# Optimization experiments

Hardware: AMD Instinct MI355X
Metric: run time of the kernel (lower is better)

The kernel has to match this reference:

```python
import jax, jax.numpy as jnp
import numpy as np

N = 50000        # node_num
E = 1600000      # num edges (avg degree 32)
IN_DIM = 128
OUT_DIM = 64
SLOPE = 0.1      # leaky relu slope_ratio
EPS = 1e-12


def setup_inputs() -> dict:
    key = jax.random.key(0)
    k0, k1, k2, k3 = jax.random.split(key, 4)
    x = jax.random.normal(k0, (N, IN_DIM), dtype=jnp.float32)
    edge_index = jax.random.randint(k1, (2, E), 0, N, dtype=jnp.int64)
    # Linear(in_dim, out_dim) params
    W = jax.random.normal(k2, (OUT_DIM, IN_DIM), dtype=jnp.float32) * (1.0 / np.sqrt(IN_DIM))
    b = jnp.zeros((OUT_DIM,), dtype=jnp.float32)
    # attention vector a: [2*out_dim, 1], kaiming-normal-ish init
    a = jax.random.normal(k3, (2 * OUT_DIM, 1), dtype=jnp.float32) * np.sqrt(2.0 / (2 * OUT_DIM))
    return {"x": x, "edge_index": edge_index, "W": W, "b": b, "a": a}


def reference(x, edge_index, W, b, a):
    # new_embeddings = Linear(x)
    new = x @ W.T + b                          # [N, OUT_DIM]
    src = edge_index[0]
    dst = edge_index[1]
    # cat(new[src], new[dst]) @ a  ==  new[src]@a_src + new[dst]@a_dst (avoids [E, 2*OUT] intermediate)
    a_src = a[:OUT_DIM, 0]                     # [OUT_DIM]
    a_dst = a[OUT_DIM:, 0]                     # [OUT_DIM]
    score = new[src] @ a_src + new[dst] @ a_dst  # [E]
    e = jnp.exp(jax.nn.leaky_relu(score, SLOPE))  # [E]
    # spmm(A, ones) -> per-row sum of edge weights; spmm(A, new) -> weighted aggregation
    row_sum = jax.ops.segment_sum(e, src, num_segments=N)                 # [N]
    results = jax.ops.segment_sum(e[:, None] * new[dst], src, num_segments=N)  # [N, OUT_DIM]
    return results / (row_sum[:, None] + EPS)
```

## Files before the change

### kernel.cpp

```cpp
#include <hip/hip_runtime.h>
#include <hip/hip_bf16.h>

#define NN    50000
#define EE    1600000
#define IND   128
#define OUTD  64
#define SLOPE 0.1f

#define BSH    5
#define BW     32
#define NB     1564
#define NFINE  1568
#define CAP    1408
#define CAPT   6
#define CSH    8
#define NC     196
#define CAP1   8832
#define NBLK1  500
#define CHUNK1 (EE / NBLK1)
#define NSPLIT 4
#define SCAP   (CAP1 / NSPLIT)
#define NLIN   (NN / 16)

typedef __attribute__((ext_vector_type(8))) short short8;
typedef __attribute__((ext_vector_type(4))) float float4v;

union SMem {
    struct {
        ushort xs[16 * 136];
        ushort wt[64 * 136];
        float  newt[16 * 68];
    } lin;
    int h[NC];
};

__global__ __launch_bounds__(256) void fused_lincoarse_kernel(
    const float* __restrict__ x, const float* __restrict__ W,
    const float* __restrict__ bias, const float* __restrict__ a,
    const int* __restrict__ ei, int* __restrict__ gcur1,
    unsigned* __restrict__ ebuf1,
    ushort* __restrict__ nbuf2, float* __restrict__ s_src, float* __restrict__ s_dst)
{
    __shared__ SMem sm;
    const int tid = threadIdx.x;

    if (blockIdx.x < NBLK1) {
        int* h = sm.h;
        for (int i = tid; i < NC; i += 256) h[i] = 0;
        __syncthreads();
        const int base = blockIdx.x * CHUNK1;
        const int4* s4p = (const int4*)(ei + base);
        for (int i = tid; i < CHUNK1 / 4; i += 256) {
            int4 s4 = s4p[i];
            atomicAdd(&h[s4.x >> CSH], 1);
            atomicAdd(&h[s4.y >> CSH], 1);
            atomicAdd(&h[s4.z >> CSH], 1);
            atomicAdd(&h[s4.w >> CSH], 1);
        }
        __syncthreads();
        for (int i = tid; i < NC; i += 256) {
            int c = h[i];
            if (c) h[i] = i * CAP1 + atomicAdd(&gcur1[i * 16], c);
        }
        __syncthreads();
        const int4* d4p = (const int4*)(ei + EE + base);
        for (int i = tid; i < CHUNK1 / 4; i += 256) {
            int4 s4 = s4p[i];
            int4 d4 = d4p[i];
            int p0 = atomicAdd(&h[s4.x >> CSH], 1);
            int p1 = atomicAdd(&h[s4.y >> CSH], 1);
            int p2 = atomicAdd(&h[s4.z >> CSH], 1);
            int p3 = atomicAdd(&h[s4.w >> CSH], 1);
            ebuf1[p0] = ((unsigned)(s4.x & 255) << 16) | (unsigned)d4.x;
            ebuf1[p1] = ((unsigned)(s4.y & 255) << 16) | (unsigned)d4.y;
            ebuf1[p2] = ((unsigned)(s4.z & 255) << 16) | (unsigned)d4.z;
            ebuf1[p3] = ((unsigned)(s4.w & 255) << 16) | (unsigned)d4.w;
        }
        return;
    }

    const int node0 = (blockIdx.x - NBLK1) * 16;
    const float4* W4 = (const float4*)W;
    #pragma unroll
    for (int i = 0; i < 8; ++i) {
        int idx = tid + i * 256;
        float4 wv = W4[idx];
        int n = idx >> 5, k = (idx & 31) * 4;
        ushort4 pk; __hip_bfloat16 h;
        h = __float2bfloat16(wv.x); pk.x = *(ushort*)&h;
        h = __float2bfloat16(wv.y); pk.y = *(ushort*)&h;
        h = __float2bfloat16(wv.z); pk.z = *(ushort*)&h;
        h = __float2bfloat16(wv.w); pk.w = *(ushort*)&h;
        *(ushort4*)&sm.lin.wt[n * 136 + k] = pk;
    }
    const float4* x4 = (const float4*)(x + (size_t)node0 * IND);
    #pragma unroll
    for (int i = 0; i < 2; ++i) {
        int idx = tid + i * 256;
        float4 xv = x4[idx];
        int r = idx >> 5, cc = (idx & 31) * 4;
        ushort4 pk; __hip_bfloat16 h;
        h = __float2bfloat16(xv.x); pk.x = *(ushort*)&h;
        h = __float2bfloat16(xv.y); pk.y = *(ushort*)&h;
        h = __float2bfloat16(xv.z); pk.z = *(ushort*)&h;
        h = __float2bfloat16(xv.w); pk.w = *(ushort*)&h;
        *(ushort4*)&sm.lin.xs[r * 136 + cc] = pk;
    }
    __syncthreads();

    const int w    = tid >> 6;
    const int lane = tid & 63;
    const int q    = lane >> 4;
    const int m16  = lane & 15;
    float4v acc = {0.f, 0.f, 0.f, 0.f};
    #pragma unroll
    for (int kk = 0; kk < IND; kk += 32) {
        short8 af = *(const short8*)&sm.lin.xs[m16 * 136 + kk + q * 8];
        short8 bf = *(const short8*)&sm.lin.wt[(w * 16 + m16) * 136 + kk + q * 8];
        acc = __builtin_amdgcn_mfma_f32_16x16x32_bf16(af, bf, acc, 0, 0, 0);
    }
    const float bv = bias[w * 16 + m16];
    #pragma unroll
    for (int r = 0; r < 4; ++r)
        sm.lin.newt[(q * 4 + r) * 68 + w * 16 + m16] = acc[r] + bv;
    __syncthreads();

    const int nl = tid >> 4;
    const int jg = tid & 15;
    const int j0 = jg * 4;
    float4 va = *(const float4*)&sm.lin.newt[nl * 68 + j0];
    const int n = node0 + nl;
    ushort4 pk;
    { __hip_bfloat16 h;
      h = __float2bfloat16(va.x); pk.x = *(ushort*)&h;
      h = __float2bfloat16(va.y); pk.y = *(ushort*)&h;
      h = __float2bfloat16(va.z); pk.z = *(ushort*)&h;
      h = __float2bfloat16(va.w); pk.w = *(ushort*)&h; }
    *(ushort4*)&nbuf2[(size_t)n * OUTD + j0] = pk;

    float ss = va.x * a[j0]        + va.y * a[j0 + 1]
             + va.z * a[j0 + 2]    + va.w * a[j0 + 3];
    float sd = va.x * a[OUTD + j0]     + va.y * a[OUTD + j0 + 1]
             + va.z * a[OUTD + j0 + 2] + va.w * a[OUTD + j0 + 3];
    #pragma unroll
    for (int m = 1; m < 16; m <<= 1) {
        ss += __shfl_xor(ss, m, 64);
        sd += __shfl_xor(sd, m, 64);
    }
    if (jg == 0) { s_src[n] = ss; s_dst[n] = sd; }
}

__global__ __launch_bounds__(256) void finebin_kernel(
    const unsigned* __restrict__ ebuf1, const int* __restrict__ gcur1,
    int* __restrict__ gcur2, unsigned* __restrict__ ebuf2)
{
    __shared__ unsigned stage[SCAP];
    __shared__ int h[8], lofs[8], grun[8], cur[8];
    const int tid = threadIdx.x;
    const int c   = blockIdx.x >> 2;
    const int sp  = blockIdx.x & 3;
    const int cnt1 = gcur1[c * 16];
    const int seg  = (cnt1 + NSPLIT - 1) / NSPLIT;
    const int lo   = sp * seg;
    const int m    = max(0, min(cnt1, lo + seg) - lo);
    if (tid < 8) h[tid] = 0;
    __syncthreads();
    const unsigned* eb = ebuf1 + (size_t)c * CAP1 + lo;
    for (int i = tid; i < m; i += 256)
        atomicAdd(&h[eb[i] >> 21], 1);
    __syncthreads();
    if (tid == 0) {
        int run = 0;
        #pragma unroll
        for (int f = 0; f < 8; ++f) { lofs[f] = run; run += h[f]; }
    }
    __syncthreads();
    if (tid < 8) {
        cur[tid]  = lofs[tid];
        grun[tid] = atomicAdd(&gcur2[(c * 8 + tid) * 16], h[tid]);
    }
    __syncthreads();
    for (int i = tid; i < m; i += 256) {
        unsigned e = eb[i];
        int pos = atomicAdd(&cur[e >> 21], 1);
        stage[pos] = (((e >> 16) & 31u) << 16) | (e & 0xFFFFu);
    }
    __syncthreads();
    #pragma unroll 1
    for (int f = 0; f < 8; ++f) {
        const int cf = h[f];
        unsigned* dst = ebuf2 + (size_t)(c * 8 + f) * CAP + grun[f];
        const unsigned* sp2 = stage + lofs[f];
        for (int i = tid; i < cf; i += 256) dst[i] = sp2[i];
    }
}

__global__ __launch_bounds__(256) void aggregate_kernel(
    const unsigned* __restrict__ ebuf, const int* __restrict__ gcur,
    const ushort* __restrict__ nbuf2,
    const float* __restrict__ s_src, const float* __restrict__ s_dst,
    float* __restrict__ out)
{
    __shared__ uint2 pairs[CAP];
    __shared__ float ssL[BW];
    __shared__ int cntL[BW], ofs[BW], cur[BW];
    const int tid  = threadIdx.x;
    const int wid  = tid >> 6;
    const int lane = tid & 63;
    const int b    = blockIdx.x;
    const int n0   = b << BSH;
    const uint2* __restrict__ nbufq = (const uint2*)nbuf2;

    if (tid < BW) {
        int n = n0 + tid;
        ssL[tid]  = (n < NN) ? s_src[n] : 0.f;
        cntL[tid] = 0;
    }
    __syncthreads();

    const int cnt = gcur[b * 16];
    const unsigned* eb = ebuf + (size_t)b * CAP;

    unsigned er[CAPT]; float evr[CAPT];
    int nk = 0;
    for (int i = tid; i < cnt; i += 256) {
        unsigned e = eb[i];
        int d  = e & 0xFFFFu;
        int ln = e >> 16;
        float sc = ssL[ln] + s_dst[d];
        float lr = sc > 0.f ? sc : SLOPE * sc;
        er[nk] = e; evr[nk] = __expf(lr); ++nk;
        atomicAdd(&cntL[ln], 1);
    }
    __syncthreads();

    if (wid == 0) {
        int c = (lane < BW) ? cntL[lane] : 0;
        int sc = c;
        #pragma unroll
        for (int m = 1; m < BW; m <<= 1) {
            int v = __shfl_up(sc, m, 64);
            if (lane >= m) sc += v;
        }
        if (lane < BW) { ofs[lane] = sc - c; cur[lane] = sc - c; }
    }
    __syncthreads();

    for (int k = 0; k < nk; ++k) {
        int ln = er[k] >> 16;
        int pos = atomicAdd(&cur[ln], 1);
        pairs[pos] = make_uint2(er[k] & 0xFFFFu, __float_as_uint(evr[k]));
    }
    __syncthreads();

    const int e16 = lane >> 4;
    const int c16 = lane & 15;

    #pragma unroll 1
    for (int t = 0; t < BW / 4; ++t) {
        const int ln  = wid * (BW / 4) + t;
        const int beg = ofs[ln];
        const int len = cntL[ln];

        float a0 = 0.f, a1 = 0.f, a2 = 0.f, a3 = 0.f, es = 0.f;
        int j = 0;
        for (; j + 16 <= len; j += 16) {
            uint2 pA = pairs[beg + j + 0  + e16];
            uint2 pB = pairs[beg + j + 4  + e16];
            uint2 pC = pairs[beg + j + 8  + e16];
            uint2 pD = pairs[beg + j + 12 + e16];
            uint2 gA = nbufq[pA.x * 16 + c16];
            uint2 gB = nbufq[pB.x * 16 + c16];
            uint2 gC = nbufq[pC.x * 16 + c16];
            uint2 gD = nbufq[pD.x * 16 + c16];
            float fA = __uint_as_float(pA.y), fB = __uint_as_float(pB.y);
            float fC = __uint_as_float(pC.y), fD = __uint_as_float(pD.y);
            es += fA + fB + fC + fD;
            a0 = fmaf(fA, __uint_as_float(gA.x << 16), a0);
            a1 = fmaf(fA, __uint_as_float(gA.x & 0xFFFF0000u), a1);
            a2 = fmaf(fA, __uint_as_float(gA.y << 16), a2);
            a3 = fmaf(fA, __uint_as_float(gA.y & 0xFFFF0000u), a3);
            a0 = fmaf(fB, __uint_as_float(gB.x << 16), a0);
            a1 = fmaf(fB, __uint_as_float(gB.x & 0xFFFF0000u), a1);
            a2 = fmaf(fB, __uint_as_float(gB.y << 16), a2);
            a3 = fmaf(fB, __uint_as_float(gB.y & 0xFFFF0000u), a3);
            a0 = fmaf(fC, __uint_as_float(gC.x << 16), a0);
            a1 = fmaf(fC, __uint_as_float(gC.x & 0xFFFF0000u), a1);
            a2 = fmaf(fC, __uint_as_float(gC.y << 16), a2);
            a3 = fmaf(fC, __uint_as_float(gC.y & 0xFFFF0000u), a3);
            a0 = fmaf(fD, __uint_as_float(gD.x << 16), a0);
            a1 = fmaf(fD, __uint_as_float(gD.x & 0xFFFF0000u), a1);
            a2 = fmaf(fD, __uint_as_float(gD.y << 16), a2);
            a3 = fmaf(fD, __uint_as_float(gD.y & 0xFFFF0000u), a3);
        }
        for (; j < len; j += 4) {
            int idx = j + e16;
            uint2 p = pairs[beg + min(idx, len - 1)];
            float f = (idx < len) ? __uint_as_float(p.y) : 0.f;
            uint2 g = nbufq[p.x * 16 + c16];
            es += f;
            a0 = fmaf(f, __uint_as_float(g.x << 16), a0);
            a1 = fmaf(f, __uint_as_float(g.x & 0xFFFF0000u), a1);
            a2 = fmaf(f, __uint_as_float(g.y << 16), a2);
            a3 = fmaf(f, __uint_as_float(g.y & 0xFFFF0000u), a3);
        }
        es += __shfl_xor(es, 16, 64); es += __shfl_xor(es, 32, 64);
        a0 += __shfl_xor(a0, 16, 64); a0 += __shfl_xor(a0, 32, 64);
        a1 += __shfl_xor(a1, 16, 64); a1 += __shfl_xor(a1, 32, 64);
        a2 += __shfl_xor(a2, 16, 64); a2 += __shfl_xor(a2, 32, 64);
        a3 += __shfl_xor(a3, 16, 64); a3 += __shfl_xor(a3, 32, 64);
        const int n = n0 + ln;
        if (e16 == 0 && n < NN) {
            float inv = 1.f / (es + 1e-12f);
            float4 o = make_float4(a0 * inv, a1 * inv, a2 * inv, a3 * inv);
            *(float4*)&out[(size_t)n * OUTD + c16 * 4] = o;
        }
    }
}

extern "C" void kernel_launch(void* const* d_in, const int* in_sizes, int n_in,
                              void* d_out, int out_size, void* d_ws, size_t ws_size,
                              hipStream_t stream) {
    const float* x  = (const float*)d_in[0];
    const int*   ei = (const int*)d_in[1];
    const float* W  = (const float*)d_in[2];
    const float* b  = (const float*)d_in[3];
    const float* a  = (const float*)d_in[4];
    float* out = (float*)d_out;

    ushort*   nbuf2 = (ushort*)d_ws;
    float*    s_src = (float*)(nbuf2 + (size_t)NN * OUTD);
    float*    s_dst = s_src + NN;
    int*      gcur1 = (int*)(s_dst + NN);
    int*      gcur2 = gcur1 + NC * 16;
    unsigned* ebuf1 = (unsigned*)(gcur2 + NFINE * 16);
    unsigned* ebuf2 = ebuf1 + (size_t)NC * CAP1;

    hipMemsetAsync(gcur1, 0, (NC + NFINE) * 16 * sizeof(int), stream);
    fused_lincoarse_kernel<<<NBLK1 + NLIN, 256, 0, stream>>>(
        x, W, b, a, ei, gcur1, ebuf1, nbuf2, s_src, s_dst);
    finebin_kernel<<<NC * NSPLIT, 256, 0, stream>>>(ebuf1, gcur1, gcur2, ebuf2);
    aggregate_kernel<<<NB, 256, 0, stream>>>(ebuf2, gcur2, nbuf2, s_src, s_dst, out);
}
```

Before: 146.6 us.

## Fold fine binning into aggregation by filtering coarse bins per block

Removes the separate fine-binning kernel and its intermediate edge buffer. Each aggregation block now scans the whole coarse bin (eight blocks' worth of edges) twice and keeps only edges matching its sub-bin. This saves one launch, one global write and read of the edge buffer, and a memset, at the cost of reading each coarse bin eight times over and doing redundant filtering work per block.

Measured after the change: 156.6 us. 6.8% more time.

```diff
diff --git a/kernel.cpp b/kernel.cpp
--- a/kernel.cpp
+++ b/kernel.cpp
@@ -10,16 +10,12 @@
 #define BSH    5
 #define BW     32
 #define NB     1564
-#define NFINE  1568
 #define CAP    1408
-#define CAPT   6
 #define CSH    8
 #define NC     196
 #define CAP1   8832
 #define NBLK1  500
 #define CHUNK1 (EE / NBLK1)
-#define NSPLIT 4
-#define SCAP   (CAP1 / NSPLIT)
 #define NLIN   (NN / 16)
 
 typedef __attribute__((ext_vector_type(8))) short short8;
@@ -150,53 +146,8 @@
     if (jg == 0) { s_src[n] = ss; s_dst[n] = sd; }
 }
 
-__global__ __launch_bounds__(256) void finebin_kernel(
+__global__ __launch_bounds__(256) void aggregate_kernel(
     const unsigned* __restrict__ ebuf1, const int* __restrict__ gcur1,
-    int* __restrict__ gcur2, unsigned* __restrict__ ebuf2)
-{
-    __shared__ unsigned stage[SCAP];
-    __shared__ int h[8], lofs[8], grun[8], cur[8];
-    const int tid = threadIdx.x;
-    const int c   = blockIdx.x >> 2;
-    const int sp  = blockIdx.x & 3;
-    const int cnt1 = gcur1[c * 16];
-    const int seg  = (cnt1 + NSPLIT - 1) / NSPLIT;
-    const int lo   = sp * seg;
-    const int m    = max(0, min(cnt1, lo + seg) - lo);
-    if (tid < 8) h[tid] = 0;
-    __syncthreads();
-    const unsigned* eb = ebuf1 + (size_t)c * CAP1 + lo;
-    for (int i = tid; i < m; i += 256)
-        atomicAdd(&h[eb[i] >> 21], 1);
-    __syncthreads();
-    if (tid == 0) {
-        int run = 0;
-        #pragma unroll
-        for (int f = 0; f < 8; ++f) { lofs[f] = run; run += h[f]; }
-    }
-    __syncthreads();
-    if (tid < 8) {
-        cur[tid]  = lofs[tid];
-        grun[tid] = atomicAdd(&gcur2[(c * 8 + tid) * 16], h[tid]);
-    }
-    __syncthreads();
-    for (int i = tid; i < m; i += 256) {
-        unsigned e = eb[i];
-        int pos = atomicAdd(&cur[e >> 21], 1);
-        stage[pos] = (((e >> 16) & 31u) << 16) | (e & 0xFFFFu);
-    }
-    __syncthreads();
-    #pragma unroll 1
-    for (int f = 0; f < 8; ++f) {
-        const int cf = h[f];
-        unsigned* dst = ebuf2 + (size_t)(c * 8 + f) * CAP + grun[f];
-        const unsigned* sp2 = stage + lofs[f];
-        for (int i = tid; i < cf; i += 256) dst[i] = sp2[i];
-    }
-}
-
-__global__ __launch_bounds__(256) void aggregate_kernel(
-    const unsigned* __restrict__ ebuf, const int* __restrict__ gcur,
     const ushort* __restrict__ nbuf2,
     const float* __restrict__ s_src, const float* __restrict__ s_dst,
     float* __restrict__ out)
@@ -208,6 +159,8 @@
     const int wid  = tid >> 6;
     const int lane = tid & 63;
     const int b    = blockIdx.x;
+    const int c    = b >> 3;
+    const unsigned fsub = (unsigned)(b & 7);
     const int n0   = b << BSH;
     const uint2* __restrict__ nbufq = (const uint2*)nbuf2;
 
@@ -218,38 +171,46 @@
     }
     __syncthreads();
 
-    const int cnt = gcur[b * 16];
-    const unsigned* eb = ebuf + (size_t)b * CAP;
-
-    unsigned er[CAPT]; float evr[CAPT];
-    int nk = 0;
-    for (int i = tid; i < cnt; i += 256) {
+    const int cnt1 = gcur1[c * 16];
+    const unsigned* eb = ebuf1 + (size_t)c * CAP1;
+
+    const int nv = cnt1 >> 2;
+    const uint4* eb4 = (const uint4*)eb;
+    for (int i = tid; i < nv; i += 256) {
+        uint4 e4 = eb4[i];
+        if ((e4.x >> 21) == fsub) atomicAdd(&cntL[(e4.x >> 16) & 31], 1);
+        if ((e4.y >> 21) == fsub) atomicAdd(&cntL[(e4.y >> 16) & 31], 1);
+        if ((e4.z >> 21) == fsub) atomicAdd(&cntL[(e4.z >> 16) & 31], 1);
+        if ((e4.w >> 21) == fsub) atomicAdd(&cntL[(e4.w >> 16) & 31], 1);
+    }
+    for (int i = (nv << 2) + tid; i < cnt1; i += 256) {
         unsigned e = eb[i];
-        int d  = e & 0xFFFFu;
-        int ln = e >> 16;
-        float sc = ssL[ln] + s_dst[d];
-        float lr = sc > 0.f ? sc : SLOPE * sc;
-        er[nk] = e; evr[nk] = __expf(lr); ++nk;
-        atomicAdd(&cntL[ln], 1);
+        if ((e >> 21) == fsub) atomicAdd(&cntL[(e >> 16) & 31], 1);
     }
     __syncthreads();
 
     if (wid == 0) {
-        int c = (lane < BW) ? cntL[lane] : 0;
-        int sc = c;
+        int cc = (lane < BW) ? cntL[lane] : 0;
+        int sc = cc;
         #pragma unroll
         for (int m = 1; m < BW; m <<= 1) {
             int v = __shfl_up(sc, m, 64);
             if (lane >= m) sc += v;
         }
-        if (lane < BW) { ofs[lane] = sc - c; cur[lane] = sc - c; }
-    }
-    __syncthreads();
-
-    for (int k = 0; k < nk; ++k) {
-        int ln = er[k] >> 16;
+        if (lane < BW) { ofs[lane] = sc - cc; cur[lane] = sc - cc; }
+    }
+    __syncthreads();
+
+    for (int i = tid; i < cnt1; i += 256) {
+        unsigned e = eb[i];
+        if ((e >> 21) != fsub) continue;
+        int d  = e & 0xFFFFu;
+        int ln = (e >> 16) & 31;
+        float sc = ssL[ln] + s_dst[d];
+        float lr = sc > 0.f ? sc : SLOPE * sc;
+        float ev = __expf(lr);
         int pos = atomicAdd(&cur[ln], 1);
-        pairs[pos] = make_uint2(er[k] & 0xFFFFu, __float_as_uint(evr[k]));
+        pairs[pos] = make_uint2((unsigned)d, __float_as_uint(ev));
     }
     __syncthreads();
 
@@ -332,13 +293,10 @@
     float*    s_src = (float*)(nbuf2 + (size_t)NN * OUTD);
     float*    s_dst = s_src + NN;
     int*      gcur1 = (int*)(s_dst + NN);
-    int*      gcur2 = gcur1 + NC * 16;
-    unsigned* ebuf1 = (unsigned*)(gcur2 + NFINE * 16);
-    unsigned* ebuf2 = ebuf1 + (size_t)NC * CAP1;
-
-    hipMemsetAsync(gcur1, 0, (NC + NFINE) * 16 * sizeof(int), stream);
+    unsigned* ebuf1 = (unsigned*)(gcur1 + NC * 16);
+
+    hipMemsetAsync(gcur1, 0, NC * 16 * sizeof(int), stream);
     fused_lincoarse_kernel<<<NBLK1 + NLIN, 256, 0, stream>>>(
         x, W, b, a, ei, gcur1, ebuf1, nbuf2, s_src, s_dst);
-    finebin_kernel<<<NC * NSPLIT, 256, 0, stream>>>(ebuf1, gcur1, gcur2, ebuf2);
-    aggregate_kernel<<<NB, 256, 0, stream>>>(ebuf2, gcur2, nbuf2, s_src, s_dst, out);
+    aggregate_kernel<<<NB, 256, 0, stream>>>(ebuf1, gcur1, nbuf2, s_src, s_dst, out);
 }
```
